# Optimization experiments

Hardware: AMD Instinct MI355X
Metric: run time of the kernel (lower is better)

The kernel has to match this reference:

```python
import jax, jax.numpy as jnp
import numpy as np

N = 50000   # num nodes
E = 400000  # num edges (avg degree 8)
D = 256     # in_channels
H = 256     # hidden_channels
C = 64      # out_channels
K = 2       # k_hops


def setup_inputs() -> dict:
    key = jax.random.key(0)
    ks = jax.random.split(key, 10)
    x = jax.random.normal(ks[0], (N, D), dtype=jnp.float32)
    edge_index = jax.random.randint(ks[1], (2, E), 0, N, dtype=jnp.int32)
    s = 0.05
    # per-hop linears of the single H2GCNConv (weights stored [in, out])
    W0 = jax.random.normal(ks[2], (D, H), jnp.float32) * s
    W1 = jax.random.normal(ks[3], (D, H), jnp.float32) * s
    W2 = jax.random.normal(ks[4], (D, H), jnp.float32) * s
    b0 = jnp.zeros((H,), jnp.float32)
    b1 = jnp.zeros((H,), jnp.float32)
    b2 = jnp.zeros((H,), jnp.float32)
    # classifier: h2_out_dim = H*(K+1) = 768 -> C
    Wc = jax.random.normal(ks[5], (H * (K + 1), C), jnp.float32) * s
    bc = jnp.zeros((C,), jnp.float32)
    return {"x": x, "edge_index": edge_index, "num_nodes": N,
            "W0": W0, "b0": b0, "W1": W1, "b1": b1, "W2": W2, "b2": b2,
            "Wc": Wc, "bc": bc}


def _normalize_adj(edge_index, num_nodes):
    # add self loops, then D^{-1/2} A D^{-1/2} edge weights
    loops = jnp.arange(num_nodes, dtype=edge_index.dtype)
    ei = jnp.concatenate([edge_index, jnp.stack([loops, loops])], axis=1)
    row, col = ei[0], ei[1]
    deg = jax.ops.segment_sum(jnp.ones(row.shape[0], jnp.float32), row,
                              num_segments=num_nodes)
    dis = jnp.where(deg > 0, deg ** -0.5, 0.0)  # inf -> 0 for isolated nodes
    return ei, dis[row] * dis[col]


def _sparse_mm(edge_index, edge_weight, x, num_nodes):
    # gather -> scale -> scatter-add (COO SpMM)
    row, col = edge_index[0], edge_index[1]
    msg = x[col] * edge_weight[:, None]  # [E', F]
    return jax.ops.segment_sum(msg, row, num_segments=num_nodes)


def reference(x, edge_index, num_nodes, W0, b0, W1, b1, W2, b2, Wc, bc):
    ei, ew = _normalize_adj(edge_index, num_nodes)
    # H2GCNConv: ego + k-hop aggregates, each through its own linear, concat
    outs = [x @ W0 + b0]
    cur = x
    for Wk, bk in ((W1, b1), (W2, b2)):
        cur = _sparse_mm(ei, ew, cur, num_nodes)
        outs.append(cur @ Wk + bk)
    h = jax.nn.relu(jnp.concatenate(outs, axis=1))  # [N, 3H]
    # dropout p=0 / eval mode -> identity
    return h @ Wc + bc
```

## Files before the change

### kernel.cpp

```cpp
#include <hip/hip_runtime.h>


#define FD 256
#define CO 64
#define SB 512
#define MT1 391
#define PS (50048 * 256)

using frag_ab = __attribute__((ext_vector_type(8))) short;
using f32x4   = __attribute__((ext_vector_type(4))) float;
typedef unsigned short u16;
typedef unsigned int   u32;

__device__ __forceinline__ u16 f2bf(float f) {
    u32 u = __builtin_bit_cast(u32, f);
    return (u16)((u + 0x7FFFu + ((u >> 16) & 1u)) >> 16);
}
__device__ __forceinline__ float bfl(u32 packed) {
    return __builtin_bit_cast(float, packed << 16);
}
__device__ __forceinline__ float bfh(u32 packed) {
    return __builtin_bit_cast(float, packed & 0xFFFF0000u);
}

__device__ __forceinline__ void gll16(const void* g, void* l) {
    __builtin_amdgcn_global_load_lds(
        (const __attribute__((address_space(1))) u32*)g,
        (__attribute__((address_space(3))) u32*)l, 16, 0, 0);
}

#define BAR()  __builtin_amdgcn_s_barrier()
#define WLG0() asm volatile("s_waitcnt lgkmcnt(0)" ::: "memory")
#define WVM0() asm volatile("s_waitcnt vmcnt(0)" ::: "memory")
#define WVM2() asm volatile("s_waitcnt vmcnt(2)" ::: "memory")

__global__ void init_kernel(int* deg, int* fill, int n) {
    int i = blockIdx.x * blockDim.x + threadIdx.x;
    if (i < n) { deg[i] = 1; fill[i] = 0; }
}
__global__ void count_kernel(const int* __restrict__ ei0, int* deg, int e) {
    int i = blockIdx.x * blockDim.x + threadIdx.x;
    if (i < e) atomicAdd(&deg[ei0[i]], 1);
}
__global__ void scan1(const int* __restrict__ deg, int* __restrict__ rowptr,
                      int* __restrict__ bsum, float* __restrict__ dis, int n) {
    __shared__ int sh[SB];
    int tid = threadIdx.x;
    int i = blockIdx.x * SB + tid;
    int v = (i < n) ? deg[i] : 0;
    if (i < n) dis[i] = rsqrtf((float)v);
    sh[tid] = v;
    __syncthreads();
    for (int off = 1; off < SB; off <<= 1) {
        int add = (tid >= off) ? sh[tid - off] : 0;
        __syncthreads();
        sh[tid] += add;
        __syncthreads();
    }
    if (i < n) rowptr[i] = sh[tid] - v;
    if (tid == SB - 1) bsum[blockIdx.x] = sh[tid];
}
__global__ void scan2(const int* __restrict__ bsum, int* __restrict__ bscan, int nb) {
    __shared__ int sh[128];
    int tid = threadIdx.x;
    int v = (tid < nb) ? bsum[tid] : 0;
    sh[tid] = v;
    __syncthreads();
    for (int off = 1; off < 128; off <<= 1) {
        int add = (tid >= off) ? sh[tid - off] : 0;
        __syncthreads();
        sh[tid] += add;
        __syncthreads();
    }
    if (tid < nb) bscan[tid] = sh[tid] - v;
    if (tid == nb - 1) bscan[nb] = sh[tid];
}
__global__ void scan3(int* rowptr, const int* __restrict__ bscan, int n, int nb) {
    int i = blockIdx.x * 256 + threadIdx.x;
    if (i < n) rowptr[i] += bscan[i / SB];
    if (i == n) rowptr[n] = bscan[nb];
}
__global__ void fill_kernel(const int* __restrict__ ei, const float* __restrict__ dis,
                            const int* __restrict__ rowptr, int* fill,
                            int2* __restrict__ cw, int e, int n) {
    int i = blockIdx.x * blockDim.x + threadIdx.x;
    if (i >= e + n) return;
    int r, c;
    if (i < e) { r = ei[i]; c = ei[e + i]; }
    else       { r = i - e; c = r; }
    float w = dis[r] * dis[c];
    int pos = rowptr[r] + atomicAdd(&fill[r], 1);
    int2 p; p.x = c; p.y = __float_as_int(w);
    cw[pos] = p;
}

__global__ void conv_kernel(const float* __restrict__ x, u16* __restrict__ xb, int total4) {
    int i = blockIdx.x * blockDim.x + threadIdx.x;
    if (i < total4) {
        float4 v = ((const float4*)x)[i];
        ushort4 o;
        o.x = f2bf(v.x); o.y = f2bf(v.y); o.z = f2bf(v.z); o.w = f2bf(v.w);
        ((ushort4*)xb)[i] = o;
    }
}
__global__ void wtrans_kernel(const float* __restrict__ W0, const float* __restrict__ W1,
                              const float* __restrict__ W2, const float* __restrict__ Wc,
                              u16* __restrict__ WkT, u16* __restrict__ WcT) {
    __shared__ u16 tl[64][65];
    int b = blockIdx.x;
    const float* src; u16* dst; int R, C, r0, c0;
    if (b < 48) {
        int k = b >> 4, t = b & 15;
        src = (k == 0) ? W0 : (k == 1) ? W1 : W2;
        dst = WkT + k * 65536;
        R = 256; C = 256; r0 = (t >> 2) * 64; c0 = (t & 3) * 64;
    } else {
        int t = b - 48;
        src = Wc; dst = WcT;
        R = 768; C = 64; r0 = t * 64; c0 = 0;
    }
    int tid = threadIdx.x;
    int rr = tid >> 4, cc = (tid & 15) * 4;
    #pragma unroll
    for (int it = 0; it < 4; ++it) {
        int r = it * 16 + rr;
        float4 v = *(const float4*)(src + (size_t)(r0 + r) * C + c0 + cc);
        tl[cc + 0][r] = f2bf(v.x); tl[cc + 1][r] = f2bf(v.y);
        tl[cc + 2][r] = f2bf(v.z); tl[cc + 3][r] = f2bf(v.w);
    }
    __syncthreads();
    #pragma unroll
    for (int it = 0; it < 4; ++it) {
        int crow = it * 16 + rr;
        ushort4 o;
        o.x = tl[crow][cc + 0]; o.y = tl[crow][cc + 1];
        o.z = tl[crow][cc + 2]; o.w = tl[crow][cc + 3];
        *(ushort4*)(dst + (size_t)(c0 + crow) * R + r0 + cc) = o;
    }
}

__global__ void spmm_bf16(const int* __restrict__ rowptr, const int2* __restrict__ cw,
                          const u16* __restrict__ xb, u16* __restrict__ outb, int n) {
    int tid = threadIdx.x;
    int lane = tid & 63;
    int row = blockIdx.x * 8 + ((tid >> 6) << 1) + (lane >> 5);
    if (row >= n) return;
    int l32 = lane & 31;
    int p0 = rowptr[row], p1 = rowptr[row + 1];
    float a[8];
    #pragma unroll
    for (int j = 0; j < 8; ++j) a[j] = 0.f;

    int p = p0;
    for (; p + 8 <= p1; p += 8) {
        int2 cwv[8]; uint4 v[8];
        #pragma unroll
        for (int u = 0; u < 8; ++u) cwv[u] = cw[p + u];
        #pragma unroll
        for (int u = 0; u < 8; ++u)
            v[u] = *(const uint4*)(xb + (size_t)cwv[u].x * FD + l32 * 8);
        #pragma unroll
        for (int u = 0; u < 8; ++u) {
            float wt = __int_as_float(cwv[u].y);
            a[0] += wt * bfl(v[u].x); a[1] += wt * bfh(v[u].x);
            a[2] += wt * bfl(v[u].y); a[3] += wt * bfh(v[u].y);
            a[4] += wt * bfl(v[u].z); a[5] += wt * bfh(v[u].z);
            a[6] += wt * bfl(v[u].w); a[7] += wt * bfh(v[u].w);
        }
    }
    for (; p + 2 <= p1; p += 2) {
        int2 cwv[2]; uint4 v[2];
        #pragma unroll
        for (int u = 0; u < 2; ++u) cwv[u] = cw[p + u];
        #pragma unroll
        for (int u = 0; u < 2; ++u)
            v[u] = *(const uint4*)(xb + (size_t)cwv[u].x * FD + l32 * 8);
        #pragma unroll
        for (int u = 0; u < 2; ++u) {
            float wt = __int_as_float(cwv[u].y);
            a[0] += wt * bfl(v[u].x); a[1] += wt * bfh(v[u].x);
            a[2] += wt * bfl(v[u].y); a[3] += wt * bfh(v[u].y);
            a[4] += wt * bfl(v[u].z); a[5] += wt * bfh(v[u].z);
            a[6] += wt * bfl(v[u].w); a[7] += wt * bfh(v[u].w);
        }
    }
    for (; p < p1; ++p) {
        int2 cwv = cw[p];
        float wt = __int_as_float(cwv.y);
        uint4 v = *(const uint4*)(xb + (size_t)cwv.x * FD + l32 * 8);
        a[0] += wt * bfl(v.x); a[1] += wt * bfh(v.x);
        a[2] += wt * bfl(v.y); a[3] += wt * bfh(v.y);
        a[4] += wt * bfl(v.z); a[5] += wt * bfh(v.z);
        a[6] += wt * bfl(v.w); a[7] += wt * bfh(v.w);
    }
    uint4 o;
    o.x = (u32)f2bf(a[0]) | ((u32)f2bf(a[1]) << 16);
    o.y = (u32)f2bf(a[2]) | ((u32)f2bf(a[3]) << 16);
    o.z = (u32)f2bf(a[4]) | ((u32)f2bf(a[5]) << 16);
    o.w = (u32)f2bf(a[6]) | ((u32)f2bf(a[7]) << 16);
    *(uint4*)(outb + (size_t)row * FD + l32 * 8) = o;
}

__launch_bounds__(256, 2)
__global__ void gemm1(const u16* __restrict__ xb, const u16* __restrict__ agg1b,
                      const u16* __restrict__ agg2b, const u16* __restrict__ WkT,
                      const float* __restrict__ b0, const float* __restrict__ b1,
                      const float* __restrict__ b2, u16* __restrict__ T, int n) {
    __shared__ __align__(16) char lds[65536];

    const int tid = threadIdx.x;
    const int w = tid >> 6, l = tid & 63;
    const int l4 = l >> 4, lm = l & 15;
    const int mq = w & 1, nq = w >> 1;

    int bid = blockIdx.x;
    const int nt  = bid & 1;
    int rest = bid >> 1;
    const int mt  = rest % MT1;
    const int seg = rest / MT1;
    const int row0 = mt * 128;
    const int n0   = nt * 128;

    const u16* inb = (seg == 0) ? xb : (seg == 1) ? agg1b : agg2b;
    const u16* WT  = WkT + (size_t)seg * 65536;
    const float* bk = (seg == 0) ? b0 : (seg == 1) ? b1 : b2;

    auto stage = [&](int kt, char* buf) {
        #pragma unroll
        for (int c = 0; c < 4; ++c) {
            int L = w * 1024 + c * 4096 + l * 16;
            int r = L >> 7, s = (L >> 4) & 7;
            int k16 = s ^ (r & 7);
            int gr = row0 + r; if (gr > n - 1) gr = n - 1;
            gll16(inb + (size_t)gr * FD + kt * 64 + k16 * 8, buf + w * 1024 + c * 4096);
        }
        #pragma unroll
        for (int c = 0; c < 4; ++c) {
            int L = w * 1024 + c * 4096 + l * 16;
            int r = L >> 7, s = (L >> 4) & 7;
            int k16 = s ^ (r & 7);
            gll16(WT + (size_t)(n0 + r) * FD + kt * 64 + k16 * 8,
                  buf + 16384 + w * 1024 + c * 4096);
        }
    };

    f32x4 acc[4][4];
    #pragma unroll
    for (int jm = 0; jm < 4; ++jm)
        #pragma unroll
        for (int rn = 0; rn < 4; ++rn) acc[jm][rn] = (f32x4)(0.f);

    stage(0, lds);
    WVM0();
    BAR();

    #pragma unroll
    for (int kt = 0; kt < 4; ++kt) {
        char* cur = lds + (kt & 1) * 32768;
        if (kt < 3) stage(kt + 1, lds + ((kt + 1) & 1) * 32768);

        #pragma unroll
        for (int kk2 = 0; kk2 < 2; ++kk2) {
            frag_ab af[4], bf_[4];
            #pragma unroll
            for (int jm = 0; jm < 4; ++jm) {
                int rB = nq * 64 + jm * 16 + lm;
                af[jm] = *(const frag_ab*)(cur + 16384 + rB * 128 + (((kk2 * 4 + l4) ^ (rB & 7)) << 4));
            }
            #pragma unroll
            for (int rn = 0; rn < 4; ++rn) {
                int rA = mq * 64 + rn * 16 + lm;
                bf_[rn] = *(const frag_ab*)(cur + rA * 128 + (((kk2 * 4 + l4) ^ (rA & 7)) << 4));
            }
            #pragma unroll
            for (int jm = 0; jm < 4; ++jm)
                #pragma unroll
                for (int rn = 0; rn < 4; ++rn)
                    acc[jm][rn] = __builtin_amdgcn_mfma_f32_16x16x32_bf16(af[jm], bf_[rn], acc[jm][rn], 0, 0, 0);
        }

        if (kt < 3) WVM0();
        WLG0();
        BAR();
    }

    u16* Tp = T + (size_t)seg * PS;
    #pragma unroll
    for (int jm = 0; jm < 4; ++jm) {
        int j = n0 + nq * 64 + jm * 16 + l4 * 4;
        float4 bb = *(const float4*)(bk + j);
        #pragma unroll
        for (int rn = 0; rn < 4; ++rn) {
            int r = row0 + mq * 64 + rn * 16 + lm;
            f32x4 v = acc[jm][rn];
            ushort4 p;
            p.x = f2bf(fmaxf(v[0] + bb.x, 0.f));
            p.y = f2bf(fmaxf(v[1] + bb.y, 0.f));
            p.z = f2bf(fmaxf(v[2] + bb.z, 0.f));
            p.w = f2bf(fmaxf(v[3] + bb.w, 0.f));
            *(ushort4*)(Tp + (size_t)r * FD + j) = p;
        }
    }
}

__launch_bounds__(256, 3)
__global__ void gemm2(const u16* __restrict__ T, const u16* __restrict__ WcT,
                      const float* __restrict__ bc, float* __restrict__ out, int n) {
    __shared__ __align__(16) char lds[16384];
    const int tid = threadIdx.x;
    const int w = tid >> 6, l = tid & 63;
    const int l4 = l >> 4, lm = l & 15;
    const int row0 = blockIdx.x * 64;
    const int rr = w * 16 + lm;
    const int r  = row0 + rr;

    frag_ab b[24];
    #pragma unroll
    for (int kt = 0; kt < 12; ++kt)
        #pragma unroll
        for (int kk2 = 0; kk2 < 2; ++kk2)
            b[kt * 2 + kk2] = *(const frag_ab*)(T + (size_t)(kt >> 2) * PS +
                                                (size_t)r * FD + (kt & 3) * 64 + kk2 * 32 + l4 * 8);

    auto stageW = [&](int kt, char* buf) {
        #pragma unroll
        for (int i = 0; i < 2; ++i) {
            int L = tid * 16 + i * 4096;
            int c = L >> 7, s = (L >> 4) & 7;
            gll16(WcT + (size_t)c * 768 + kt * 64 + (s ^ (c & 7)) * 8,
                  buf + w * 1024 + i * 4096);
        }
    };

    f32x4 acc[4];
    #pragma unroll
    for (int am = 0; am < 4; ++am) acc[am] = (f32x4)(0.f);

    stageW(0, lds);
    #pragma unroll
    for (int kt = 0; kt < 12; ++kt) {
        char* cur = lds + (kt & 1) * 8192;
        if (kt < 11) {
            stageW(kt + 1, lds + ((kt + 1) & 1) * 8192);
            WVM2();
        } else {
            WVM0();
        }
        BAR();
        #pragma unroll
        for (int kk2 = 0; kk2 < 2; ++kk2) {
            #pragma unroll
            for (int am = 0; am < 4; ++am) {
                int c = am * 16 + lm;
                frag_ab afr = *(const frag_ab*)(cur + c * 128 + (((kk2 * 4 + l4) ^ (c & 7)) << 4));
                acc[am] = __builtin_amdgcn_mfma_f32_16x16x32_bf16(afr, b[kt * 2 + kk2], acc[am], 0, 0, 0);
            }
        }
        WLG0();
        BAR();
    }

    if (r < n) {
        #pragma unroll
        for (int am = 0; am < 4; ++am) {
            float4 bb = *(const float4*)(bc + am * 16 + l4 * 4);
            float4 o;
            o.x = acc[am][0] + bb.x;
            o.y = acc[am][1] + bb.y;
            o.z = acc[am][2] + bb.z;
            o.w = acc[am][3] + bb.w;
            *(float4*)(out + (size_t)r * CO + am * 16 + l4 * 4) = o;
        }
    }
}

extern "C" void kernel_launch(void* const* d_in, const int* in_sizes, int n_in,
                              void* d_out, int out_size, void* d_ws, size_t ws_size,
                              hipStream_t stream) {
    const float* x  = (const float*)d_in[0];
    const int*   ei = (const int*)d_in[1];
    const float* W0 = (const float*)d_in[3];
    const float* b0 = (const float*)d_in[4];
    const float* W1 = (const float*)d_in[5];
    const float* b1 = (const float*)d_in[6];
    const float* W2 = (const float*)d_in[7];
    const float* b2 = (const float*)d_in[8];
    const float* Wc = (const float*)d_in[9];
    const float* bc = (const float*)d_in[10];
    float* out = (float*)d_out;

    const int n  = in_sizes[0] / FD;
    const int e  = in_sizes[1] / 2;
    const int ep = e + n;
    const int nb = (n + SB - 1) / SB;

    char* ws = (char*)d_ws;
    size_t o = 0;
    auto take = [&](size_t nbytes) -> char* {
        char* p = ws + o;
        o += (nbytes + 255) & ~(size_t)255;
        return p;
    };
    int*   deg    = (int*)  take((size_t)n * 4);
    int*   fill   = (int*)  take((size_t)n * 4);
    float* dis    = (float*)take((size_t)n * 4);
    int*   rowptr = (int*)  take((size_t)(n + 1) * 4);
    int*   bsum   = (int*)  take((size_t)(nb + 1) * 4);
    int*   bscan  = (int*)  take((size_t)(nb + 1) * 4);
    int2*  cw     = (int2*) take((size_t)ep * 8);
    u16*   xb     = (u16*)  take((size_t)n * FD * 2);
    u16*   agg1b  = (u16*)  take((size_t)n * FD * 2);
    u16*   agg2b  = (u16*)  take((size_t)n * FD * 2);
    u16*   WkT    = (u16*)  take((size_t)3 * FD * FD * 2);
    u16*   WcT    = (u16*)  take((size_t)CO * 3 * FD * 2);
    u16*   T      = (u16*)  take((size_t)3 * PS * 2);
    (void)ws_size; (void)n_in; (void)out_size;

    init_kernel <<<(n + 255) / 256, 256, 0, stream>>>(deg, fill, n);
    count_kernel<<<(e + 255) / 256, 256, 0, stream>>>(ei, deg, e);
    scan1       <<<nb, SB, 0, stream>>>(deg, rowptr, bsum, dis, n);
    scan2       <<<1, 128, 0, stream>>>(bsum, bscan, nb);
    scan3       <<<(n + 256) / 256, 256, 0, stream>>>(rowptr, bscan, n, nb);
    fill_kernel <<<(ep + 255) / 256, 256, 0, stream>>>(ei, dis, rowptr, fill, cw, e, n);

    const int total4 = n * FD / 4;
    conv_kernel  <<<(total4 + 255) / 256, 256, 0, stream>>>(x, xb, total4);
    wtrans_kernel<<<60, 256, 0, stream>>>(W0, W1, W2, Wc, WkT, WcT);

    spmm_bf16<<<(n + 7) / 8, 256, 0, stream>>>(rowptr, cw, xb, agg1b, n);
    spmm_bf16<<<(n + 7) / 8, 256, 0, stream>>>(rowptr, cw, agg1b, agg2b, n);

    gemm1<<<2 * MT1 * 3, 256, 0, stream>>>(xb, agg1b, agg2b, WkT, b0, b1, b2, T, n);
    gemm2<<<(n + 63) / 64, 256, 0, stream>>>(T, WcT, bc, out, n);
}
```

Measured before the change: 223.0 us.

## Single-buffer gemm1 LDS for higher occupancy and coalesce output through LDS

Replaces the double-buffered 64KB LDS staging in gemm1 with a single 32KB buffer. Each K-step now loads and then computes behind barriers, which lets launch bounds rise from 2 to 3 blocks per CU. The bias+ReLU epilogue writes the bf16 tile into swizzled LDS first, then stores full 16-byte row chunks to global memory for coalesced writes. The cost is losing the overlap of next-tile loads with MFMA work, which now relies on more resident blocks to hide latency, plus extra barriers.

```diff
diff --git a/kernel.cpp b/kernel.cpp
--- a/kernel.cpp
+++ b/kernel.cpp
@@ -201,12 +201,14 @@
     *(uint4*)(outb + (size_t)row * FD + l32 * 8) = o;
 }
 
-__launch_bounds__(256, 2)
+__launch_bounds__(256, 3)
 __global__ void gemm1(const u16* __restrict__ xb, const u16* __restrict__ agg1b,
                       const u16* __restrict__ agg2b, const u16* __restrict__ WkT,
                       const float* __restrict__ b0, const float* __restrict__ b1,
                       const float* __restrict__ b2, u16* __restrict__ T, int n) {
-    __shared__ __align__(16) char lds[65536];
+    __shared__ __align__(16) char lds[32768];
+    char* lA = lds;
+    char* lB = lds + 16384;
 
     const int tid = threadIdx.x;
     const int w = tid >> 6, l = tid & 63;
@@ -225,39 +227,32 @@
     const u16* WT  = WkT + (size_t)seg * 65536;
     const float* bk = (seg == 0) ? b0 : (seg == 1) ? b1 : b2;
 
-    auto stage = [&](int kt, char* buf) {
+    f32x4 acc[4][4];
+    #pragma unroll
+    for (int jm = 0; jm < 4; ++jm)
+        #pragma unroll
+        for (int rn = 0; rn < 4; ++rn) acc[jm][rn] = (f32x4)(0.f);
+
+    for (int kt = 0; kt < 4; ++kt) {
+        WLG0();
+        BAR();
         #pragma unroll
         for (int c = 0; c < 4; ++c) {
             int L = w * 1024 + c * 4096 + l * 16;
             int r = L >> 7, s = (L >> 4) & 7;
             int k16 = s ^ (r & 7);
             int gr = row0 + r; if (gr > n - 1) gr = n - 1;
-            gll16(inb + (size_t)gr * FD + kt * 64 + k16 * 8, buf + w * 1024 + c * 4096);
+            gll16(inb + (size_t)gr * FD + kt * 64 + k16 * 8, lA + w * 1024 + c * 4096);
         }
         #pragma unroll
         for (int c = 0; c < 4; ++c) {
             int L = w * 1024 + c * 4096 + l * 16;
             int r = L >> 7, s = (L >> 4) & 7;
             int k16 = s ^ (r & 7);
-            gll16(WT + (size_t)(n0 + r) * FD + kt * 64 + k16 * 8,
-                  buf + 16384 + w * 1024 + c * 4096);
-        }
-    };
-
-    f32x4 acc[4][4];
-    #pragma unroll
-    for (int jm = 0; jm < 4; ++jm)
-        #pragma unroll
-        for (int rn = 0; rn < 4; ++rn) acc[jm][rn] = (f32x4)(0.f);
-
-    stage(0, lds);
-    WVM0();
-    BAR();
-
-    #pragma unroll
-    for (int kt = 0; kt < 4; ++kt) {
-        char* cur = lds + (kt & 1) * 32768;
-        if (kt < 3) stage(kt + 1, lds + ((kt + 1) & 1) * 32768);
+            gll16(WT + (size_t)(n0 + r) * FD + kt * 64 + k16 * 8, lB + w * 1024 + c * 4096);
+        }
+        WVM0();
+        BAR();
 
         #pragma unroll
         for (int kk2 = 0; kk2 < 2; ++kk2) {
@@ -265,12 +260,12 @@
             #pragma unroll
             for (int jm = 0; jm < 4; ++jm) {
                 int rB = nq * 64 + jm * 16 + lm;
-                af[jm] = *(const frag_ab*)(cur + 16384 + rB * 128 + (((kk2 * 4 + l4) ^ (rB & 7)) << 4));
+                af[jm] = *(const frag_ab*)(lB + rB * 128 + (((kk2 * 4 + l4) ^ (rB & 7)) << 4));
             }
             #pragma unroll
             for (int rn = 0; rn < 4; ++rn) {
                 int rA = mq * 64 + rn * 16 + lm;
-                bf_[rn] = *(const frag_ab*)(cur + rA * 128 + (((kk2 * 4 + l4) ^ (rA & 7)) << 4));
+                bf_[rn] = *(const frag_ab*)(lA + rA * 128 + (((kk2 * 4 + l4) ^ (rA & 7)) << 4));
             }
             #pragma unroll
             for (int jm = 0; jm < 4; ++jm)
@@ -278,27 +273,37 @@
                 for (int rn = 0; rn < 4; ++rn)
                     acc[jm][rn] = __builtin_amdgcn_mfma_f32_16x16x32_bf16(af[jm], bf_[rn], acc[jm][rn], 0, 0, 0);
         }
-
-        if (kt < 3) WVM0();
-        WLG0();
-        BAR();
-    }
-
-    u16* Tp = T + (size_t)seg * PS;
+    }
+    WLG0();
+    BAR();
+
     #pragma unroll
     for (int jm = 0; jm < 4; ++jm) {
-        int j = n0 + nq * 64 + jm * 16 + l4 * 4;
-        float4 bb = *(const float4*)(bk + j);
+        int j = nq * 64 + jm * 16 + l4 * 4;
+        float4 bb = *(const float4*)(bk + n0 + j);
         #pragma unroll
         for (int rn = 0; rn < 4; ++rn) {
-            int r = row0 + mq * 64 + rn * 16 + lm;
+            int r = mq * 64 + rn * 16 + lm;
             f32x4 v = acc[jm][rn];
             ushort4 p;
             p.x = f2bf(fmaxf(v[0] + bb.x, 0.f));
             p.y = f2bf(fmaxf(v[1] + bb.y, 0.f));
             p.z = f2bf(fmaxf(v[2] + bb.z, 0.f));
             p.w = f2bf(fmaxf(v[3] + bb.w, 0.f));
-            *(ushort4*)(Tp + (size_t)r * FD + j) = p;
+            *(ushort4*)(lds + r * 256 + (((j >> 3) ^ (r & 7)) << 4) + (j & 7) * 2) = p;
+        }
+    }
+    WLG0();
+    BAR();
+
+    u16* Tp = T + (size_t)seg * PS;
+    {
+        const int c16 = tid & 15;
+        #pragma unroll
+        for (int i = 0; i < 8; ++i) {
+            int r = i * 16 + (tid >> 4);
+            uint4 v = *(const uint4*)(lds + r * 256 + ((c16 ^ (r & 7)) << 4));
+            *(uint4*)(Tp + (size_t)(row0 + r) * FD + n0 + c16 * 8) = v;
         }
     }
 }
```

Result: faster. 211.0 us (-5.4%).
